# Performance work log

Measured on AMD Instinct MI355X. Metric: run time of the kernel, lower is better.

## Reference

```python
import jax, jax.numpy as jnp
import numpy as np


def setup_inputs() -> dict:
    key = jax.random.key(0)
    k1, k2 = jax.random.split(key)
    E, D, N = 1600000, 32, 100000
    e = jax.random.normal(k1, (E, D), dtype=jnp.float32)
    dst = jax.random.randint(k2, (E,), 0, N, dtype=jnp.int64)
    return {"e": e, "dst": dst, "n_nodes": N}


def reference(e, dst, n_nodes):
    # copy_e + mean reducer == segment mean of edge features over dst nodes.
    # DGL yields 0 for nodes with no in-edges.
    sums = jax.ops.segment_sum(e, dst, num_segments=n_nodes)          # [N, D]
    counts = jax.ops.segment_sum(jnp.ones((e.shape[0],), e.dtype), dst,
                                 num_segments=n_nodes)                 # [N]
    denom = jnp.maximum(counts, 1.0)[:, None]
    return sums / denom
```

## Files before the change

### kernel.cpp

```cpp
#include <hip/hip_runtime.h>


#define D_FEAT 32
#define NPB 128
#define NB_MAX 1024
#define STAGE 3200
#define CAP_LDS 2560
#define CURSOR_PAD 16

__global__ __launch_bounds__(256, 4) void bin_kernel(
    const int* __restrict__ dst,
    int* __restrict__ cursor,
    unsigned int* __restrict__ buckets,
    int E, int nb, int cap, int chunk)
{
    __shared__ int hist[NB_MAX];
    __shared__ int offs[NB_MAX];
    __shared__ int run [NB_MAX];
    __shared__ int gpos[NB_MAX];
    __shared__ unsigned int   st_rec[STAGE];
    __shared__ unsigned short st_b  [STAGE];
    __shared__ int wsum[4];

    int t = threadIdx.x;
    int cstart = blockIdx.x * chunk;
    int cn = E - cstart; if (cn > chunk) cn = chunk;
    if (cn <= 0) return;

    for (int i = t; i < nb; i += 256) hist[i] = 0;
    __syncthreads();

    int nv = cn >> 2;
    const int4* d4 = (const int4*)(dst + cstart);
    for (int i = t; i < nv; i += 256) {
        int4 d = d4[i];
        atomicAdd(&hist[d.x >> 7], 1);
        atomicAdd(&hist[d.y >> 7], 1);
        atomicAdd(&hist[d.z >> 7], 1);
        atomicAdd(&hist[d.w >> 7], 1);
    }
    for (int i = (nv << 2) + t; i < cn; i += 256)
        atomicAdd(&hist[dst[cstart + i] >> 7], 1);
    __syncthreads();

    int q = (nb + 255) >> 8;
    int lo = t * q, hi = lo + q; if (hi > nb) hi = nb;
    int sum = 0;
    for (int i = lo; i < hi; i++) sum += hist[i];
    int lane = t & 63, w = t >> 6;
    int x = sum;
    for (int off = 1; off < 64; off <<= 1) {
        int y = __shfl_up(x, off, 64);
        if (lane >= off) x += y;
    }
    if (lane == 63) wsum[w] = x;
    __syncthreads();
    int wex = 0;
    for (int u = 0; u < w; u++) wex += wsum[u];
    int ex = wex + x - sum;
    for (int i = lo; i < hi; i++) {
        offs[i] = ex;
        run[i]  = ex;
        ex += hist[i];
    }
    __syncthreads();

    int off0 = (blockIdx.x * 199) % nb;
    for (int i = t; i < nb; i += 256) {
        int ii = i + off0; if (ii >= nb) ii -= nb;
        int h = hist[ii];
        gpos[ii] = (h > 0) ? atomicAdd(&cursor[ii * CURSOR_PAD], h) : 0;
    }
    __syncthreads();

    for (int i = t; i < nv; i += 256) {
        int4 d = d4[i];
        int g = cstart + (i << 2);
        int b0 = d.x >> 7, b1 = d.y >> 7, b2 = d.z >> 7, b3 = d.w >> 7;
        int p0 = atomicAdd(&run[b0], 1);
        int p1 = atomicAdd(&run[b1], 1);
        int p2 = atomicAdd(&run[b2], 1);
        int p3 = atomicAdd(&run[b3], 1);
        st_rec[p0] = ((unsigned)(g    ) << 7) | (unsigned)(d.x & 127); st_b[p0] = (unsigned short)b0;
        st_rec[p1] = ((unsigned)(g + 1) << 7) | (unsigned)(d.y & 127); st_b[p1] = (unsigned short)b1;
        st_rec[p2] = ((unsigned)(g + 2) << 7) | (unsigned)(d.z & 127); st_b[p2] = (unsigned short)b2;
        st_rec[p3] = ((unsigned)(g + 3) << 7) | (unsigned)(d.w & 127); st_b[p3] = (unsigned short)b3;
    }
    for (int i = (nv << 2) + t; i < cn; i += 256) {
        int g = cstart + i;
        int d = dst[g];
        int b = d >> 7;
        int p = atomicAdd(&run[b], 1);
        st_rec[p] = ((unsigned)g << 7) | (unsigned)(d & 127);
        st_b[p]   = (unsigned short)b;
    }
    __syncthreads();

    for (int p = t; p < cn; p += 256) {
        int b = st_b[p];
        int rel = gpos[b] + (p - offs[b]);
        if (rel < cap)
            buckets[(size_t)b * cap + rel] = st_rec[p];
    }
}

__global__ __launch_bounds__(256, 4) void bucket_gather_kernel(
    const float4* __restrict__ e4,
    const unsigned int* __restrict__ buckets,
    const int* __restrict__ cursor,
    float4* __restrict__ out4,
    int N, int cap)
{
    __shared__ unsigned int st_raw[CAP_LDS];
    __shared__ unsigned int st_srt[CAP_LDS];
    __shared__ float sums[NPB][33];
    __shared__ int hist[NPB];
    __shared__ int run [NPB];

    int t = threadIdx.x;
    int b = blockIdx.x;

    for (int i = t; i < NPB; i += 256) hist[i] = 0;
    for (int i = t; i < NPB * 33; i += 256) ((float*)sums)[i] = 0.f;
    __syncthreads();

    int m = cursor[b * CURSOR_PAD]; if (m > cap) m = cap;
    const unsigned int* rec = buckets + (size_t)b * cap;

    for (int i = t; i < m; i += 256) {
        unsigned r = rec[i];
        st_raw[i] = r;
        atomicAdd(&hist[r & 127], 1);
    }
    __syncthreads();

    if (t < 64) {
        int v0 = hist[2 * t], v1 = hist[2 * t + 1];
        int s = v0 + v1;
        int x = s;
        for (int off = 1; off < 64; off <<= 1) {
            int y = __shfl_up(x, off, 64);
            if (t >= off) x += y;
        }
        int ex = x - s;
        run[2 * t]     = ex;
        run[2 * t + 1] = ex + v0;
    }
    __syncthreads();

    for (int i = t; i < m; i += 256) {
        unsigned r = st_raw[i];
        int p = atomicAdd(&run[r & 127], 1);
        st_srt[p] = r;
    }
    __syncthreads();

    int g = t >> 3, j = t & 7;
    int slice = (m + 31) >> 5;
    int s0 = g * slice;
    int s1 = s0 + slice; if (s1 > m) s1 = m;
    float* srow = &sums[0][0] + j * 4;
    float4 acc = {0.f, 0.f, 0.f, 0.f};
    int cur = -1;
    int k = s0;
    for (; k + 4 <= s1; k += 4) {
        unsigned r0 = st_srt[k], r1 = st_srt[k+1], r2 = st_srt[k+2], r3 = st_srt[k+3];
        float4 v0 = e4[(size_t)(r0 >> 7) * 8 + j];
        float4 v1 = e4[(size_t)(r1 >> 7) * 8 + j];
        float4 v2 = e4[(size_t)(r2 >> 7) * 8 + j];
        float4 v3 = e4[(size_t)(r3 >> 7) * 8 + j];
        int l0 = r0 & 127, l1 = r1 & 127, l2 = r2 & 127, l3 = r3 & 127;
        if (l0 != cur) {
            if (cur >= 0) {
                float* p = srow + cur * 33;
                atomicAdd(p + 0, acc.x); atomicAdd(p + 1, acc.y);
                atomicAdd(p + 2, acc.z); atomicAdd(p + 3, acc.w);
            }
            acc.x = acc.y = acc.z = acc.w = 0.f; cur = l0;
        }
        acc.x += v0.x; acc.y += v0.y; acc.z += v0.z; acc.w += v0.w;
        if (l1 != cur) {
            float* p = srow + cur * 33;
            atomicAdd(p + 0, acc.x); atomicAdd(p + 1, acc.y);
            atomicAdd(p + 2, acc.z); atomicAdd(p + 3, acc.w);
            acc.x = acc.y = acc.z = acc.w = 0.f; cur = l1;
        }
        acc.x += v1.x; acc.y += v1.y; acc.z += v1.z; acc.w += v1.w;
        if (l2 != cur) {
            float* p = srow + cur * 33;
            atomicAdd(p + 0, acc.x); atomicAdd(p + 1, acc.y);
            atomicAdd(p + 2, acc.z); atomicAdd(p + 3, acc.w);
            acc.x = acc.y = acc.z = acc.w = 0.f; cur = l2;
        }
        acc.x += v2.x; acc.y += v2.y; acc.z += v2.z; acc.w += v2.w;
        if (l3 != cur) {
            float* p = srow + cur * 33;
            atomicAdd(p + 0, acc.x); atomicAdd(p + 1, acc.y);
            atomicAdd(p + 2, acc.z); atomicAdd(p + 3, acc.w);
            acc.x = acc.y = acc.z = acc.w = 0.f; cur = l3;
        }
        acc.x += v3.x; acc.y += v3.y; acc.z += v3.z; acc.w += v3.w;
    }
    for (; k < s1; k++) {
        unsigned r0 = st_srt[k];
        float4 v0 = e4[(size_t)(r0 >> 7) * 8 + j];
        int l0 = r0 & 127;
        if (l0 != cur) {
            if (cur >= 0) {
                float* p = srow + cur * 33;
                atomicAdd(p + 0, acc.x); atomicAdd(p + 1, acc.y);
                atomicAdd(p + 2, acc.z); atomicAdd(p + 3, acc.w);
            }
            acc.x = acc.y = acc.z = acc.w = 0.f; cur = l0;
        }
        acc.x += v0.x; acc.y += v0.y; acc.z += v0.z; acc.w += v0.w;
    }
    if (cur >= 0) {
        float* p = srow + cur * 33;
        atomicAdd(p + 0, acc.x); atomicAdd(p + 1, acc.y);
        atomicAdd(p + 2, acc.z); atomicAdd(p + 3, acc.w);
    }
    __syncthreads();

    for (int s = t; s < NPB * 8; s += 256) {
        int local = s >> 3, jj = s & 7;
        int node = b * NPB + local;
        if (node < N) {
            int c = hist[local];
            float inv = 1.0f / (float)(c > 1 ? c : 1);
            float4 r;
            r.x = sums[local][jj * 4 + 0] * inv;
            r.y = sums[local][jj * 4 + 1] * inv;
            r.z = sums[local][jj * 4 + 2] * inv;
            r.w = sums[local][jj * 4 + 3] * inv;
            out4[(size_t)node * 8 + jj] = r;
        }
    }
}

__global__ __launch_bounds__(256) void scatter_atomic_kernel(
    const float4* __restrict__ e4, const int* __restrict__ dst,
    float* __restrict__ sums, int* __restrict__ counts, int total)
{
    int t = blockIdx.x * 256 + threadIdx.x;
    if (t >= total) return;
    int edge = t >> 3;
    int fq = t & 7;
    float4 v = e4[t];
    int d = dst[edge];
    float* o = sums + (size_t)d * D_FEAT + fq * 4;
    atomicAdd(o + 0, v.x);
    atomicAdd(o + 1, v.y);
    atomicAdd(o + 2, v.z);
    atomicAdd(o + 3, v.w);
    if (fq == 0) atomicAdd(counts + d, 1);
}

__global__ __launch_bounds__(256) void finalize_kernel(
    float4* __restrict__ out4, const int* __restrict__ counts, int total)
{
    int t = blockIdx.x * 256 + threadIdx.x;
    if (t >= total) return;
    int node = t >> 3;
    int c = counts[node];
    float inv = 1.0f / (float)(c > 1 ? c : 1);
    float4 v = out4[t];
    v.x *= inv; v.y *= inv; v.z *= inv; v.w *= inv;
    out4[t] = v;
}

extern "C" void kernel_launch(void* const* d_in, const int* in_sizes, int n_in,
                              void* d_out, int out_size, void* d_ws, size_t ws_size,
                              hipStream_t stream) {
    const float4* e4 = (const float4*)d_in[0];
    const int* dst = (const int*)d_in[1];
    int E = in_sizes[0] / D_FEAT;
    int N = out_size / D_FEAT;

    int nb = (N + NPB - 1) / NPB;
    long long avg = (E + nb - 1) / nb;
    long long thresh = avg + 8 * (long long)(__builtin_sqrt((double)avg)) + 64;
    int cap = (int)((thresh + 63) / 64 * 64);

    char* ws = (char*)d_ws;
    size_t fast_need = (size_t)nb * CURSOR_PAD * 4
                     + (size_t)nb * cap * 4;

    if (nb <= NB_MAX && cap <= CAP_LDS && E <= (1 << 25) && ws_size >= fast_need) {
        int* cursor = (int*)ws;
        unsigned int* buckets = (unsigned int*)(ws + (size_t)nb * CURSOR_PAD * 4);

        hipMemsetAsync(cursor, 0, (size_t)nb * CURSOR_PAD * 4, stream);

        int chunk = (E + 511) / 512;
        chunk = (chunk + 3) & ~3;
        if (chunk > STAGE) chunk = STAGE & ~3;
        int grid1 = (E + chunk - 1) / chunk;
        bin_kernel<<<grid1, 256, 0, stream>>>(dst, cursor, buckets, E, nb, cap, chunk);
        bucket_gather_kernel<<<nb, 256, 0, stream>>>(e4, buckets, cursor,
                                                     (float4*)d_out, N, cap);
    } else {
        int* counts = (int*)ws;
        hipMemsetAsync(d_out, 0, (size_t)out_size * sizeof(float), stream);
        hipMemsetAsync(counts, 0, (size_t)N * 4, stream);
        int total = E * (D_FEAT / 4);
        scatter_atomic_kernel<<<(total + 255) / 256, 256, 0, stream>>>(
            e4, dst, (float*)d_out, counts, total);
        int fin = N * (D_FEAT / 4);
        finalize_kernel<<<(fin + 255) / 256, 256, 0, stream>>>(
            (float4*)d_out, counts, fin);
    }
}
```

Baseline: 335.3 us.

## Double gather block threads, drop LDS staging copy, unroll gathers by eight

The bucket gather kernel now runs 512 threads per block, so each block has 64 edge slices instead of 32. It also deepens the unroll to eight outstanding float4 loads per thread. The raw record staging array is removed, and records are re-read from global memory in the second pass, which frees LDS for more resident blocks. The fast path's edge limit is tightened to 2^24 so the packed record still fits. The aim is more memory-level parallelism for the latency-bound gather, at the cost of more LDS atomic flushes at slice boundaries and a second global read of the records.

```diff
diff --git a/kernel.cpp b/kernel.cpp
--- a/kernel.cpp
+++ b/kernel.cpp
@@ -104,14 +104,27 @@
     }
 }
 
-__global__ __launch_bounds__(256, 4) void bucket_gather_kernel(
+#define CONSUME(r, v)                                                          \
+    {                                                                          \
+        int l = (int)((r) & 127);                                              \
+        if (l != cur) {                                                        \
+            if (cur >= 0) {                                                    \
+                float* p = srow + cur * 33;                                    \
+                atomicAdd(p + 0, acc.x); atomicAdd(p + 1, acc.y);              \
+                atomicAdd(p + 2, acc.z); atomicAdd(p + 3, acc.w);              \
+            }                                                                  \
+            acc.x = acc.y = acc.z = acc.w = 0.f; cur = l;                      \
+        }                                                                      \
+        acc.x += (v).x; acc.y += (v).y; acc.z += (v).z; acc.w += (v).w;        \
+    }
+
+__global__ __launch_bounds__(512, 6) void bucket_gather_kernel(
     const float4* __restrict__ e4,
     const unsigned int* __restrict__ buckets,
     const int* __restrict__ cursor,
     float4* __restrict__ out4,
     int N, int cap)
 {
-    __shared__ unsigned int st_raw[CAP_LDS];
     __shared__ unsigned int st_srt[CAP_LDS];
     __shared__ float sums[NPB][33];
     __shared__ int hist[NPB];
@@ -120,18 +133,15 @@
     int t = threadIdx.x;
     int b = blockIdx.x;
 
-    for (int i = t; i < NPB; i += 256) hist[i] = 0;
-    for (int i = t; i < NPB * 33; i += 256) ((float*)sums)[i] = 0.f;
+    for (int i = t; i < NPB; i += 512) hist[i] = 0;
+    for (int i = t; i < NPB * 33; i += 512) ((float*)sums)[i] = 0.f;
     __syncthreads();
 
     int m = cursor[b * CURSOR_PAD]; if (m > cap) m = cap;
     const unsigned int* rec = buckets + (size_t)b * cap;
 
-    for (int i = t; i < m; i += 256) {
-        unsigned r = rec[i];
-        st_raw[i] = r;
-        atomicAdd(&hist[r & 127], 1);
-    }
+    for (int i = t; i < m; i += 512)
+        atomicAdd(&hist[rec[i] & 127], 1);
     __syncthreads();
 
     if (t < 64) {
@@ -148,72 +158,39 @@
     }
     __syncthreads();
 
-    for (int i = t; i < m; i += 256) {
-        unsigned r = st_raw[i];
+    for (int i = t; i < m; i += 512) {
+        unsigned r = rec[i];
         int p = atomicAdd(&run[r & 127], 1);
         st_srt[p] = r;
     }
     __syncthreads();
 
     int g = t >> 3, j = t & 7;
-    int slice = (m + 31) >> 5;
+    int slice = (m + 63) >> 6;
     int s0 = g * slice;
     int s1 = s0 + slice; if (s1 > m) s1 = m;
     float* srow = &sums[0][0] + j * 4;
     float4 acc = {0.f, 0.f, 0.f, 0.f};
     int cur = -1;
     int k = s0;
-    for (; k + 4 <= s1; k += 4) {
-        unsigned r0 = st_srt[k], r1 = st_srt[k+1], r2 = st_srt[k+2], r3 = st_srt[k+3];
+    for (; k + 8 <= s1; k += 8) {
+        unsigned r0 = st_srt[k],   r1 = st_srt[k+1], r2 = st_srt[k+2], r3 = st_srt[k+3];
+        unsigned r4 = st_srt[k+4], r5 = st_srt[k+5], r6 = st_srt[k+6], r7 = st_srt[k+7];
         float4 v0 = e4[(size_t)(r0 >> 7) * 8 + j];
         float4 v1 = e4[(size_t)(r1 >> 7) * 8 + j];
         float4 v2 = e4[(size_t)(r2 >> 7) * 8 + j];
         float4 v3 = e4[(size_t)(r3 >> 7) * 8 + j];
-        int l0 = r0 & 127, l1 = r1 & 127, l2 = r2 & 127, l3 = r3 & 127;
-        if (l0 != cur) {
-            if (cur >= 0) {
-                float* p = srow + cur * 33;
-                atomicAdd(p + 0, acc.x); atomicAdd(p + 1, acc.y);
-                atomicAdd(p + 2, acc.z); atomicAdd(p + 3, acc.w);
-            }
-            acc.x = acc.y = acc.z = acc.w = 0.f; cur = l0;
-        }
-        acc.x += v0.x; acc.y += v0.y; acc.z += v0.z; acc.w += v0.w;
-        if (l1 != cur) {
-            float* p = srow + cur * 33;
-            atomicAdd(p + 0, acc.x); atomicAdd(p + 1, acc.y);
-            atomicAdd(p + 2, acc.z); atomicAdd(p + 3, acc.w);
-            acc.x = acc.y = acc.z = acc.w = 0.f; cur = l1;
-        }
-        acc.x += v1.x; acc.y += v1.y; acc.z += v1.z; acc.w += v1.w;
-        if (l2 != cur) {
-            float* p = srow + cur * 33;
-            atomicAdd(p + 0, acc.x); atomicAdd(p + 1, acc.y);
-            atomicAdd(p + 2, acc.z); atomicAdd(p + 3, acc.w);
-            acc.x = acc.y = acc.z = acc.w = 0.f; cur = l2;
-        }
-        acc.x += v2.x; acc.y += v2.y; acc.z += v2.z; acc.w += v2.w;
-        if (l3 != cur) {
-            float* p = srow + cur * 33;
-            atomicAdd(p + 0, acc.x); atomicAdd(p + 1, acc.y);
-            atomicAdd(p + 2, acc.z); atomicAdd(p + 3, acc.w);
-            acc.x = acc.y = acc.z = acc.w = 0.f; cur = l3;
-        }
-        acc.x += v3.x; acc.y += v3.y; acc.z += v3.z; acc.w += v3.w;
+        float4 v4 = e4[(size_t)(r4 >> 7) * 8 + j];
+        float4 v5 = e4[(size_t)(r5 >> 7) * 8 + j];
+        float4 v6 = e4[(size_t)(r6 >> 7) * 8 + j];
+        float4 v7 = e4[(size_t)(r7 >> 7) * 8 + j];
+        CONSUME(r0, v0); CONSUME(r1, v1); CONSUME(r2, v2); CONSUME(r3, v3);
+        CONSUME(r4, v4); CONSUME(r5, v5); CONSUME(r6, v6); CONSUME(r7, v7);
     }
     for (; k < s1; k++) {
         unsigned r0 = st_srt[k];
         float4 v0 = e4[(size_t)(r0 >> 7) * 8 + j];
-        int l0 = r0 & 127;
-        if (l0 != cur) {
-            if (cur >= 0) {
-                float* p = srow + cur * 33;
-                atomicAdd(p + 0, acc.x); atomicAdd(p + 1, acc.y);
-                atomicAdd(p + 2, acc.z); atomicAdd(p + 3, acc.w);
-            }
-            acc.x = acc.y = acc.z = acc.w = 0.f; cur = l0;
-        }
-        acc.x += v0.x; acc.y += v0.y; acc.z += v0.z; acc.w += v0.w;
+        CONSUME(r0, v0);
     }
     if (cur >= 0) {
         float* p = srow + cur * 33;
@@ -222,7 +199,7 @@
     }
     __syncthreads();
 
-    for (int s = t; s < NPB * 8; s += 256) {
+    for (int s = t; s < NPB * 8; s += 512) {
         int local = s >> 3, jj = s & 7;
         int node = b * NPB + local;
         if (node < N) {
@@ -286,7 +263,7 @@
     size_t fast_need = (size_t)nb * CURSOR_PAD * 4
                      + (size_t)nb * cap * 4;
 
-    if (nb <= NB_MAX && cap <= CAP_LDS && E <= (1 << 25) && ws_size >= fast_need) {
+    if (nb <= NB_MAX && cap <= CAP_LDS && E <= (1 << 24) && ws_size >= fast_need) {
         int* cursor = (int*)ws;
         unsigned int* buckets = (unsigned int*)(ws + (size_t)nb * CURSOR_PAD * 4);
 
@@ -297,7 +274,7 @@
         if (chunk > STAGE) chunk = STAGE & ~3;
         int grid1 = (E + chunk - 1) / chunk;
         bin_kernel<<<grid1, 256, 0, stream>>>(dst, cursor, buckets, E, nb, cap, chunk);
-        bucket_gather_kernel<<<nb, 256, 0, stream>>>(e4, buckets, cursor,
+        bucket_gather_kernel<<<nb, 512, 0, stream>>>(e4, buckets, cursor,
                                                      (float4*)d_out, N, cap);
     } else {
         int* counts = (int*)ws;
```

After: 332.3 us. About the same (-0.9%).
